# Kernel tuning notes

Hardware: AMD Instinct MI355X
Metric: run time of the kernel (lower is better)

## Reference

```python
import jax, jax.numpy as jnp
from jax import lax
import numpy as np

BN_EPS = 1e-5
LEAKY_SLOPE = 0.1


def _conv(x, w, stride=1):
    # x: [B,Cin,H,W], w: [Cout,Cin,kh,kw], 'same' padding (padding = k//2)
    p = w.shape[2] // 2
    return lax.conv_general_dilated(x, w, (stride, stride), [(p, p), (p, p)],
                                    dimension_numbers=('NCHW', 'OIHW', 'NCHW'))


def _bn(x, g, b, m, v):
    scale = g / jnp.sqrt(v + BN_EPS)
    return x * scale[None, :, None, None] + (b - m * scale)[None, :, None, None]


def _leaky(x):
    return jnp.where(x >= 0, x, LEAKY_SLOPE * x)


def _identity_grid(s, dtype=jnp.float32):
    # F.affine_grid identity, align_corners=True: grid[i,j] = (x_j, y_i), coords in [-1,1]
    xs = jnp.linspace(-1.0, 1.0, s, dtype=dtype)
    gx, gy = jnp.meshgrid(xs, xs)  # gx[i,j]=xs[j], gy[i,j]=xs[i]
    return jnp.stack([gx, gy], axis=-1)[None]  # [1,s,s,2]


def _grid_sample(img, grid):
    # torch.nn.functional.grid_sample, bilinear, align_corners=True, padding_mode='zeros'
    # img: [B,C,H,W], grid: [B,h,w,2] with grid[...,0]=x(width), grid[...,1]=y(height)
    B, C, H, W = img.shape
    x = (grid[..., 0] + 1.0) * 0.5 * (W - 1)
    y = (grid[..., 1] + 1.0) * 0.5 * (H - 1)
    x0f = jnp.floor(x)
    y0f = jnp.floor(y)
    x0 = x0f.astype(jnp.int32)
    y0 = y0f.astype(jnp.int32)
    x1 = x0 + 1
    y1 = y0 + 1
    wx1 = x - x0f
    wx0 = 1.0 - wx1
    wy1 = y - y0f
    wy0 = 1.0 - wy1

    def corner(xi, yi, w):
        m = ((xi >= 0) & (xi < W) & (yi >= 0) & (yi < H)).astype(img.dtype)
        xc = jnp.clip(xi, 0, W - 1)
        yc = jnp.clip(yi, 0, H - 1)
        gath = jax.vmap(lambda im, yy, xx: im[:, yy, xx])(img, yc, xc)  # [B,C,h,w]
        return gath * (w * m)[:, None]

    return (corner(x0, y0, wx0 * wy0) + corner(x1, y0, wx1 * wy0) +
            corner(x0, y1, wx0 * wy1) + corner(x1, y1, wx1 * wy1))


def _correlation(tgt_list, src_list):
    # corr[b, t, h, w] = sum_c tgt[b,c,t] * src[b,c,(h,w)], concat over feature layers (dim 1)
    outs = []
    for t, s in zip(tgt_list, src_list):
        B, C, H, W = t.shape
        c = jnp.einsum('bct,bcs->bts', t.reshape(B, C, H * W), s.reshape(B, C, H * W))
        outs.append(c.reshape(B, H * W, H, W))
    return jnp.concatenate(outs, axis=1)


def _stn_block(corr, i, w0, bn0_g, bn0_b, bn0_m, bn0_v, w1, bn1_g, bn1_b, bn1_m, bn1_v,
               w2, bn2_g, bn2_b, bn2_m, bn2_v, w3, b3):
    # downscale_factor == 1 (output_size == input_size), upsample-to-same-size is identity
    x = _leaky(_bn(_conv(corr, w0[i], stride=1), bn0_g[i], bn0_b[i], bn0_m[i], bn0_v[i]))
    x = _leaky(_bn(_conv(x, w1[i]), bn1_g[i], bn1_b[i], bn1_m[i], bn1_v[i]))
    x = _leaky(_bn(_conv(x, w2[i]), bn2_g[i], bn2_b[i], bn2_m[i], bn2_v[i]))
    x = _conv(x, w3[i]) + b3[i][None, :, None, None]
    return x  # [B,2,S,S]


def setup_inputs() -> dict:
    key = jax.random.key(0)
    ks = iter(jax.random.split(key, 16))
    B, C, S, L, NS = 8, 256, 32, 2, 3  # batch, feat channels, spatial, n feature layers, n scales
    HW = S * S
    d = {
        'src_layer2': jax.random.normal(next(ks), (B, C, S, S), jnp.float32) * 0.1,
        'src_layer3': jax.random.normal(next(ks), (B, C, S, S), jnp.float32) * 0.1,
        'tgt_layer2': jax.random.normal(next(ks), (B, C, S, S), jnp.float32) * 0.1,
        'tgt_layer3': jax.random.normal(next(ks), (B, C, S, S), jnp.float32) * 0.1,
        'w0': jax.random.normal(next(ks), (NS, HW, HW * L, 1, 1), jnp.float32) * 0.02,
        'w1': jax.random.normal(next(ks), (NS, HW // 2, HW, 3, 3), jnp.float32) * 0.02,
        'w2': jax.random.normal(next(ks), (NS, HW // 4, HW // 2, 3, 3), jnp.float32) * 0.02,
        'w3': jax.random.normal(next(ks), (NS, 2, HW // 4, 1, 1), jnp.float32) * 0.02,
        'b3': jnp.zeros((NS, 2), jnp.float32),
    }
    for j, ch in [(0, HW), (1, HW // 2), (2, HW // 4)]:
        d[f'bn{j}_g'] = jnp.ones((NS, ch), jnp.float32)
        d[f'bn{j}_b'] = jnp.zeros((NS, ch), jnp.float32)
        d[f'bn{j}_m'] = jnp.zeros((NS, ch), jnp.float32)
        d[f'bn{j}_v'] = jnp.ones((NS, ch), jnp.float32)
    return d


def reference(src_layer2, src_layer3, tgt_layer2, tgt_layer3,
              w0, bn0_g, bn0_b, bn0_m, bn0_v,
              w1, bn1_g, bn1_b, bn1_m, bn1_v,
              w2, bn2_g, bn2_b, bn2_m, bn2_v,
              w3, b3):
    src = [src_layer2, src_layer3]
    tgt = [tgt_layer2, tgt_layer3]
    S = src_layer2.shape[-1]
    ident = _identity_grid(S, src_layer2.dtype)  # [1,S,S,2]
    params = (w0, bn0_g, bn0_b, bn0_m, bn0_v, w1, bn1_g, bn1_b, bn1_m, bn1_v,
              w2, bn2_g, bn2_b, bn2_m, bn2_v, w3, b3)

    corr = _correlation(tgt, src)
    flow = jnp.transpose(_stn_block(corr, 0, *params), (0, 2, 3, 1)) + ident  # [B,S,S,2]
    n_scales = w0.shape[0]
    for i in range(1, n_scales):
        warped = [_grid_sample(s, flow) for s in src]
        corr = _correlation(tgt, warped)
        flow = flow + jnp.transpose(_stn_block(corr, i, *params), (0, 2, 3, 1))
    return flow
```

## Files before the change

kernel.cpp:

```cpp
#include <hip/hip_runtime.h>
#include <cstdint>
#include <cstddef>


typedef unsigned short u16;
using bf16x8 = __attribute__((ext_vector_type(8))) short;
using f32x4  = __attribute__((ext_vector_type(4))) float;

constexpr float BN_EPS = 1e-5f;
constexpr float SLOPE  = 0.1f;

__device__ __forceinline__ u16 f2bf(float f) {
    union { float f; uint32_t u; } c; c.f = f;
    uint32_t u = c.u;
    return (u16)((u + 0x7fffu + ((u >> 16) & 1u)) >> 16);
}
__device__ __forceinline__ float bf2f(u16 h) {
    union { uint32_t u; float f; } c; c.u = ((uint32_t)h) << 16;
    return c.f;
}

#define MFMA16(a, b, c) __builtin_amdgcn_mfma_f32_16x16x32_bf16(a, b, c, 0, 0, 0)

constexpr size_t OFF_TGT2B  = 0;
constexpr size_t OFF_TGT3B  = 2097152;
constexpr size_t OFF_SRCT2  = 4194304;
constexpr size_t OFF_SRCT3  = 6291456;
constexpr size_t OFF_WARPT2 = 8388608;
constexpr size_t OFF_WARPT3 = 10485760;
constexpr size_t OFF_WPK1   = 12582912;
constexpr size_t OFF_WPK2   = 17301504;
constexpr size_t OFF_EX1    = 18481152;
constexpr size_t OFF_X0P    = 23216128;
constexpr size_t OFF_FLOW   = 32686080;

__global__ __launch_bounds__(256) void cvt_kernel(
    const float* __restrict__ in, u16* __restrict__ out, int n)
{
    int i = (blockIdx.x * 256 + threadIdx.x) * 4;
    if (i + 3 < n) {
        float4 v = *(const float4*)(in + i);
        ushort4 o;
        o.x = f2bf(v.x); o.y = f2bf(v.y); o.z = f2bf(v.z); o.w = f2bf(v.w);
        *(ushort4*)(out + i) = o;
    }
}

__global__ __launch_bounds__(256) void transpose_cvt(
    const float* __restrict__ in, u16* __restrict__ out)
{
    __shared__ float tile[32][33];
    const int s0 = blockIdx.x * 32;
    const int c0 = blockIdx.y * 32;
    const int b  = blockIdx.z;
    const int tid = threadIdx.x;
    const int tx = tid & 31, ty = tid >> 5;
    const float* ib = in + ((size_t)b * 256 + c0) * 1024 + s0;
    #pragma unroll
    for (int r = 0; r < 4; ++r)
        tile[ty + r * 8][tx] = ib[(size_t)(ty + r * 8) * 1024 + tx];
    __syncthreads();
    u16* ob = out + ((size_t)b * 1024 + s0) * 256 + c0;
    #pragma unroll
    for (int r = 0; r < 4; ++r) {
        int s = ty + r * 8;
        ob[(size_t)s * 256 + tx] = f2bf(tile[tx][s]);
    }
}

__global__ __launch_bounds__(256) void pack_conv_w(
    const float* __restrict__ w, u16* __restrict__ out, int COUT, int CIN)
{
    int idx = blockIdx.x * 256 + threadIdx.x;
    if (idx >= COUT * CIN) return;
    int o = idx / CIN, c = idx - o * CIN;
    const float* g = w + (size_t)idx * 9;
    u16* ob = out + (size_t)o * 9 * CIN + c;
    #pragma unroll
    for (int t = 0; t < 9; ++t) ob[(size_t)t * CIN] = f2bf(g[t]);
}

template<int C>
__global__ __launch_bounds__(256) void zero_pads(u16* __restrict__ xP)
{
    constexpr int NC = C / 8;
    int idx = blockIdx.x * 256 + threadIdx.x;
    if (idx >= 8 * 132 * NC) return;
    int c8  = idx & (NC - 1);
    int rem = idx / NC;
    int b = rem / 132, j = rem - b * 132;
    int pos;
    if (j < 34)      pos = j;
    else if (j < 68) pos = 1122 + (j - 34);
    else { int k = j - 68; pos = ((k >> 1) + 1) * 34 + (k & 1) * 33; }
    *(bf16x8*)&xP[((size_t)b * 1156 + pos) * C + c8 * 8] = (bf16x8){0,0,0,0,0,0,0,0};
}

__global__ __launch_bounds__(256) void e_gemm(
    const u16* __restrict__ w0b,
    const u16* __restrict__ tgt2b,
    const u16* __restrict__ tgt3b,
    u16* __restrict__ E)
{
    __shared__ u16 ash[128 * 64];
    __shared__ u16 bsh[128 * 64];
    const int c0 = blockIdx.x * 128;
    const int o0 = blockIdx.y * 128;
    const int b  = blockIdx.z >> 1;
    const int l  = blockIdx.z & 1;
    const u16* tgt = (l == 0 ? tgt2b : tgt3b) + (size_t)b * 262144;
    const int tid = threadIdx.x, lane = tid & 63, wid = tid >> 6;
    const int wm = (wid >> 1) * 64, wn = (wid & 1) * 64;

    f32x4 acc[4][4];
    #pragma unroll
    for (int i = 0; i < 4; ++i)
        #pragma unroll
        for (int j = 0; j < 4; ++j) acc[i][j] = (f32x4){0.f, 0.f, 0.f, 0.f};

    for (int k0 = 0; k0 < 1024; k0 += 64) {
        #pragma unroll
        for (int p = 0; p < 4; ++p) {
            int idx = p * 256 + tid;
            int row = idx >> 3, s = idx & 7;
            *(bf16x8*)&ash[row * 64 + ((s ^ (row & 7)) << 3)] =
                *(const bf16x8*)(w0b + (size_t)(o0 + row) * 2048 + l * 1024 + k0 + s * 8);
            *(bf16x8*)&bsh[row * 64 + ((s ^ (row & 7)) << 3)] =
                *(const bf16x8*)(tgt + (size_t)(c0 + row) * 1024 + k0 + s * 8);
        }
        __syncthreads();
        #pragma unroll
        for (int kk = 0; kk < 2; ++kk) {
            bf16x8 af[4], bfr[4];
            #pragma unroll
            for (int i = 0; i < 4; ++i) {
                int row = wm + i * 16 + (lane & 15);
                int s = kk * 4 + (lane >> 4);
                af[i] = *(const bf16x8*)&ash[row * 64 + ((s ^ (row & 7)) << 3)];
                int rowb = wn + i * 16 + (lane & 15);
                bfr[i] = *(const bf16x8*)&bsh[rowb * 64 + ((s ^ (rowb & 7)) << 3)];
            }
            #pragma unroll
            for (int i = 0; i < 4; ++i)
                #pragma unroll
                for (int j = 0; j < 4; ++j)
                    acc[i][j] = MFMA16(af[i], bfr[j], acc[i][j]);
        }
        __syncthreads();
    }
    u16* Eb = E + ((size_t)blockIdx.z * 1024 + o0) * 256 + c0;
    #pragma unroll
    for (int i = 0; i < 4; ++i)
        #pragma unroll
        for (int j = 0; j < 4; ++j)
            #pragma unroll
            for (int r = 0; r < 4; ++r) {
                int m = wm + i * 16 + ((lane >> 4) << 2) + r;
                int n = wn + j * 16 + (lane & 15);
                Eb[(size_t)m * 256 + n] = f2bf(acc[i][j][r]);
            }
}

__global__ __launch_bounds__(256) void x0_gemm(
    const u16* __restrict__ sA2,
    const u16* __restrict__ sA3,
    const u16* __restrict__ E,
    const float* __restrict__ bng, const float* __restrict__ bnb,
    const float* __restrict__ bnm, const float* __restrict__ bnv,
    u16* __restrict__ x0P)
{
    __shared__ u16 ash[128 * 64];
    __shared__ u16 bsh[128 * 64];
    const int o0 = blockIdx.x * 128;
    const int s0 = blockIdx.y * 128;
    const int b  = blockIdx.z;
    const int tid = threadIdx.x, lane = tid & 63, wid = tid >> 6;
    const int wm = (wid >> 1) * 64, wn = (wid & 1) * 64;

    f32x4 acc[4][4];
    #pragma unroll
    for (int i = 0; i < 4; ++i)
        #pragma unroll
        for (int j = 0; j < 4; ++j) acc[i][j] = (f32x4){0.f, 0.f, 0.f, 0.f};

    for (int kc = 0; kc < 8; ++kc) {
        const int l = kc >> 2;
        const int c0k = (kc & 3) * 64;
        const u16* sa = (l == 0 ? sA2 : sA3) + (size_t)b * 262144;
        const u16* eb = E + (size_t)((b << 1) + l) * 262144;
        #pragma unroll
        for (int p = 0; p < 4; ++p) {
            int idx = p * 256 + tid;
            int row = idx >> 3, s = idx & 7;
            *(bf16x8*)&ash[row * 64 + ((s ^ (row & 7)) << 3)] =
                *(const bf16x8*)(sa + (size_t)(s0 + row) * 256 + c0k + s * 8);
            *(bf16x8*)&bsh[row * 64 + ((s ^ (row & 7)) << 3)] =
                *(const bf16x8*)(eb + (size_t)(o0 + row) * 256 + c0k + s * 8);
        }
        __syncthreads();
        #pragma unroll
        for (int kk = 0; kk < 2; ++kk) {
            bf16x8 af[4], bfr[4];
            #pragma unroll
            for (int i = 0; i < 4; ++i) {
                int row = wm + i * 16 + (lane & 15);
                int s = kk * 4 + (lane >> 4);
                af[i] = *(const bf16x8*)&ash[row * 64 + ((s ^ (row & 7)) << 3)];
                int rowb = wn + i * 16 + (lane & 15);
                bfr[i] = *(const bf16x8*)&bsh[rowb * 64 + ((s ^ (rowb & 7)) << 3)];
            }
            #pragma unroll
            for (int i = 0; i < 4; ++i)
                #pragma unroll
                for (int j = 0; j < 4; ++j)
                    acc[i][j] = MFMA16(af[i], bfr[j], acc[i][j]);
        }
        __syncthreads();
    }
    #pragma unroll
    for (int j = 0; j < 4; ++j) {
        const int o = o0 + wn + j * 16 + (lane & 15);
        const float scv = bng[o] * rsqrtf(bnv[o] + BN_EPS);
        const float shv = bnb[o] - bnm[o] * scv;
        #pragma unroll
        for (int i = 0; i < 4; ++i)
            #pragma unroll
            for (int r = 0; r < 4; ++r) {
                int m = s0 + wm + i * 16 + ((lane >> 4) << 2) + r;
                float t = acc[i][j][r] * scv + shv;
                t = t >= 0.f ? t : SLOPE * t;
                size_t sp = (size_t)b * 1156 + ((m >> 5) + 1) * 34 + (m & 31) + 1;
                x0P[sp * 1024 + o] = f2bf(t);
            }
    }
}

template<int CIN, int COUT, int NT, bool PADOUT>
__global__ __launch_bounds__(256) void conv_gemm(
    const u16* __restrict__ xinP,
    const u16* __restrict__ wpk,
    const float* __restrict__ bng, const float* __restrict__ bnb,
    const float* __restrict__ bnm, const float* __restrict__ bnv,
    u16* __restrict__ xout)
{
    constexpr int NPOS = (NT + 2) * 34;
    constexpr int JT = NT / 2;
    __shared__ u16 ash[9 * 64 * 32];
    __shared__ u16 bsh[NPOS * 36];
    const int o0 = blockIdx.x * 64;
    const int y0 = blockIdx.y * NT;
    const int b  = blockIdx.z;
    const int tid = threadIdx.x, lane = tid & 63, wid = tid >> 6;
    const int wn = wid * (NT * 8);
    const u16* xpb = xinP + ((size_t)b * 1156 + y0 * 34) * CIN;

    f32x4 acc[4][JT];
    #pragma unroll
    for (int i = 0; i < 4; ++i)
        #pragma unroll
        for (int j = 0; j < JT; ++j) acc[i][j] = (f32x4){0.f, 0.f, 0.f, 0.f};

    for (int c0 = 0; c0 < CIN; c0 += 32) {
        #pragma unroll
        for (int p = 0; p < 9; ++p) {
            int idx = p * 256 + tid;
            int row = (idx >> 2) & 63, s = idx & 3;
            *(bf16x8*)&ash[((p * 64 + row) << 5) + ((s ^ ((row >> 1) & 3)) << 3)] =
                *(const bf16x8*)(wpk + ((size_t)(o0 + row) * 9 + p) * CIN + c0 + s * 8);
        }
        for (int idx = tid; idx < NPOS * 4; idx += 256) {
            int pos = idx >> 2, s = idx & 3;
            *(bf16x8*)&bsh[pos * 36 + s * 8] =
                *(const bf16x8*)(xpb + (size_t)pos * CIN + c0 + s * 8);
        }
        __syncthreads();
        #pragma unroll
        for (int t = 0; t < 9; ++t) {
            const int dy = t / 3, dx = t - dy * 3;
            bf16x8 af[4], bfr[JT];
            #pragma unroll
            for (int i = 0; i < 4; ++i) {
                int row = i * 16 + (lane & 15);
                af[i] = *(const bf16x8*)&ash[((t * 64 + row) << 5) +
                                             (((lane >> 4) ^ ((row >> 1) & 3)) << 3)];
            }
            #pragma unroll
            for (int j = 0; j < JT; ++j) {
                int n = wn + j * 16 + (lane & 15);
                int pos = ((n >> 5) + dy) * 34 + (n & 31) + dx;
                bfr[j] = *(const bf16x8*)&bsh[pos * 36 + ((lane >> 4) << 3)];
            }
            #pragma unroll
            for (int i = 0; i < 4; ++i)
                #pragma unroll
                for (int j = 0; j < JT; ++j)
                    acc[i][j] = MFMA16(af[i], bfr[j], acc[i][j]);
        }
        __syncthreads();
    }
    #pragma unroll
    for (int i = 0; i < 4; ++i) {
        float scv[4], shv[4];
        #pragma unroll
        for (int r = 0; r < 4; ++r) {
            int o = o0 + i * 16 + ((lane >> 4) << 2) + r;
            float s = bng[o] * rsqrtf(bnv[o] + BN_EPS);
            scv[r] = s; shv[r] = bnb[o] - bnm[o] * s;
        }
        #pragma unroll
        for (int j = 0; j < JT; ++j) {
            int n = wn + j * 16 + (lane & 15);
            int yg = y0 + (n >> 5), xg = n & 31;
            size_t sp = PADOUT ? ((size_t)b * 1156 + (size_t)(yg + 1) * 34 + xg + 1)
                               : ((size_t)b * 1024 + (size_t)yg * 32 + xg);
            ushort4 pk;
            float t0 = acc[i][j][0] * scv[0] + shv[0]; t0 = t0 >= 0.f ? t0 : SLOPE * t0;
            float t1 = acc[i][j][1] * scv[1] + shv[1]; t1 = t1 >= 0.f ? t1 : SLOPE * t1;
            float t2 = acc[i][j][2] * scv[2] + shv[2]; t2 = t2 >= 0.f ? t2 : SLOPE * t2;
            float t3 = acc[i][j][3] * scv[3] + shv[3]; t3 = t3 >= 0.f ? t3 : SLOPE * t3;
            pk.x = f2bf(t0); pk.y = f2bf(t1); pk.z = f2bf(t2); pk.w = f2bf(t3);
            *(ushort4*)&xout[sp * COUT + o0 + i * 16 + ((lane >> 4) << 2)] = pk;
        }
    }
}

__global__ __launch_bounds__(64) void warp_kernel(
    const u16* __restrict__ srcT,
    const float* __restrict__ flow,
    u16* __restrict__ outT)
{
    const int bs = blockIdx.x;
    const int b = bs >> 10;
    const float fx = flow[(size_t)bs * 2 + 0];
    const float fy = flow[(size_t)bs * 2 + 1];
    const float px = (fx + 1.f) * 15.5f;
    const float py = (fy + 1.f) * 15.5f;
    const float x0f = floorf(px), y0f = floorf(py);
    const int x0 = (int)x0f, y0 = (int)y0f;
    const float wx1 = px - x0f, wx0 = 1.f - wx1;
    const float wy1 = py - y0f, wy0 = 1.f - wy1;
    const int lane = threadIdx.x;
    const u16* sb = srcT + (size_t)b * 262144 + lane * 4;
    float a0 = 0.f, a1 = 0.f, a2 = 0.f, a3 = 0.f;
    #pragma unroll
    for (int cr = 0; cr < 4; ++cr) {
        const int xi = x0 + (cr & 1), yi = y0 + (cr >> 1);
        const float w = (cr == 0 ? wx0 * wy0 : cr == 1 ? wx1 * wy0 :
                         cr == 2 ? wx0 * wy1 : wx1 * wy1);
        if (xi >= 0 && xi < 32 && yi >= 0 && yi < 32) {
            const ushort4 v = *(const ushort4*)(sb + (size_t)(yi * 32 + xi) * 256);
            a0 += w * bf2f(v.x); a1 += w * bf2f(v.y);
            a2 += w * bf2f(v.z); a3 += w * bf2f(v.w);
        }
    }
    ushort4 o;
    o.x = f2bf(a0); o.y = f2bf(a1); o.z = f2bf(a2); o.w = f2bf(a3);
    *(ushort4*)(outT + (size_t)bs * 256 + lane * 4) = o;
}

__global__ __launch_bounds__(256) void conv3_flow(
    const u16* __restrict__ x2T,
    const float* __restrict__ w3s,
    const float* __restrict__ b3s,
    float* __restrict__ flow, int add_ident)
{
    const int widx = blockIdx.x * 4 + (threadIdx.x >> 6);
    const int lane = threadIdx.x & 63;
    const ushort4 v = *(const ushort4*)&x2T[(size_t)widx * 256 + lane * 4];
    float a0 = 0.f, a1 = 0.f;
    const u16* vp = (const u16*)&v;
    #pragma unroll
    for (int j = 0; j < 4; ++j) {
        const float xv = bf2f(vp[j]);
        a0 += xv * w3s[lane * 4 + j];
        a1 += xv * w3s[256 + lane * 4 + j];
    }
    #pragma unroll
    for (int off = 32; off > 0; off >>= 1) {
        a0 += __shfl_down(a0, off);
        a1 += __shfl_down(a1, off);
    }
    if (lane == 0) {
        a0 += b3s[0]; a1 += b3s[1];
        float* f = flow + (size_t)widx * 2;
        if (add_ident) {
            const int s = widx & 1023;
            const int yy = s >> 5, xx = s & 31;
            f[0] = a0 + (-1.f + xx * (2.f / 31.f));
            f[1] = a1 + (-1.f + yy * (2.f / 31.f));
        } else {
            f[0] += a0;
            f[1] += a1;
        }
    }
}

__global__ __launch_bounds__(256) void copy_flow_kernel(
    const float* __restrict__ flow, float* __restrict__ out, int n)
{
    const int i = blockIdx.x * 256 + threadIdx.x;
    if (i < n) out[i] = flow[i];
}

extern "C" void kernel_launch(void* const* d_in, const int* in_sizes, int n_in,
                              void* d_out, int out_size, void* d_ws, size_t ws_size,
                              hipStream_t stream) {
    (void)in_sizes; (void)n_in; (void)ws_size;
    const float* src2 = (const float*)d_in[0];
    const float* src3 = (const float*)d_in[1];
    const float* tgt2 = (const float*)d_in[2];
    const float* tgt3 = (const float*)d_in[3];
    const float* w0   = (const float*)d_in[4];
    const float* w1   = (const float*)d_in[5];
    const float* w2   = (const float*)d_in[6];
    const float* w3   = (const float*)d_in[7];
    const float* b3   = (const float*)d_in[8];
    const float* bn0g = (const float*)d_in[9];
    const float* bn0b = (const float*)d_in[10];
    const float* bn0m = (const float*)d_in[11];
    const float* bn0v = (const float*)d_in[12];
    const float* bn1g = (const float*)d_in[13];
    const float* bn1b = (const float*)d_in[14];
    const float* bn1m = (const float*)d_in[15];
    const float* bn1v = (const float*)d_in[16];
    const float* bn2g = (const float*)d_in[17];
    const float* bn2b = (const float*)d_in[18];
    const float* bn2m = (const float*)d_in[19];
    const float* bn2v = (const float*)d_in[20];

    u16* ws = (u16*)d_ws;
    u16* tgt2b  = ws + OFF_TGT2B;
    u16* tgt3b  = ws + OFF_TGT3B;
    u16* srcT2  = ws + OFF_SRCT2;
    u16* srcT3  = ws + OFF_SRCT3;
    u16* warpT2 = ws + OFF_WARPT2;
    u16* warpT3 = ws + OFF_WARPT3;
    u16* wpk1   = ws + OFF_WPK1;
    u16* wpk2   = ws + OFF_WPK2;
    u16* E      = ws + OFF_EX1;
    u16* x1P    = ws + OFF_EX1;
    u16* x0P    = ws + OFF_X0P;
    u16* w0b    = ws + OFF_X0P;
    u16* x2T    = ws + OFF_WARPT2;
    float* flow = (float*)(ws + OFF_FLOW);

    cvt_kernel<<<2048, 256, 0, stream>>>(tgt2, tgt2b, 2097152);
    cvt_kernel<<<2048, 256, 0, stream>>>(tgt3, tgt3b, 2097152);
    transpose_cvt<<<dim3(32, 8, 8), 256, 0, stream>>>(src2, srcT2);
    transpose_cvt<<<dim3(32, 8, 8), 256, 0, stream>>>(src3, srcT3);

    for (int sc = 0; sc < 3; ++sc) {
        cvt_kernel<<<2048, 256, 0, stream>>>(w0 + (size_t)sc * 2097152, w0b, 2097152);
        pack_conv_w<<<2048, 256, 0, stream>>>(w1 + (size_t)sc * 4718592, wpk1, 512, 1024);
        pack_conv_w<<<512, 256, 0, stream>>>(w2 + (size_t)sc * 1179648, wpk2, 256, 512);

        const u16* a2 = srcT2;
        const u16* a3 = srcT3;
        if (sc > 0) {
            warp_kernel<<<8192, 64, 0, stream>>>(srcT2, flow, warpT2);
            warp_kernel<<<8192, 64, 0, stream>>>(srcT3, flow, warpT3);
            a2 = warpT2; a3 = warpT3;
        }
        e_gemm<<<dim3(2, 8, 16), 256, 0, stream>>>(w0b, tgt2b, tgt3b, E);
        zero_pads<1024><<<528, 256, 0, stream>>>(x0P);
        x0_gemm<<<dim3(8, 8, 8), 256, 0, stream>>>(a2, a3, E,
            bn0g + sc * 1024, bn0b + sc * 1024, bn0m + sc * 1024, bn0v + sc * 1024, x0P);
        zero_pads<512><<<264, 256, 0, stream>>>(x1P);
        conv_gemm<1024, 512, 4, true><<<dim3(8, 8, 8), 256, 0, stream>>>(x0P, wpk1,
            bn1g + sc * 512, bn1b + sc * 512, bn1m + sc * 512, bn1v + sc * 512, x1P);
        conv_gemm<512, 256, 2, false><<<dim3(4, 16, 8), 256, 0, stream>>>(x1P, wpk2,
            bn2g + sc * 256, bn2b + sc * 256, bn2m + sc * 256, bn2v + sc * 256, x2T);
        conv3_flow<<<2048, 256, 0, stream>>>(x2T, w3 + sc * 512, b3 + sc * 2,
                                             flow, sc == 0 ? 1 : 0);
    }
    copy_flow_kernel<<<64, 256, 0, stream>>>(flow, (float*)d_out, out_size);
}
```

Measured before the change: 806.4 us.

## Register-prefetch next K-chunk in conv_gemm and retile conv2 output channels

The conv_gemm main loop now loads the next 32-channel slice of weights and activations into registers while MFMAs run on the current slice in shared memory. This hides global-load latency behind compute, and the trailing barrier is replaced by one at the start of each iteration. A template parameter for the output-channel tile size is added, and conv2 switches from 64x2-row tiles to 32-channel x 4-row tiles. The change raises register pressure, which could reduce occupancy.

After: 736.0 us. -8.7%, faster.

```diff
diff --git a/kernel.cpp b/kernel.cpp
--- a/kernel.cpp
+++ b/kernel.cpp
@@ -235,7 +235,7 @@
     }
 }
 
-template<int CIN, int COUT, int NT, bool PADOUT>
+template<int CIN, int COUT, int MB, int NT, bool PADOUT>
 __global__ __launch_bounds__(256) void conv_gemm(
     const u16* __restrict__ xinP,
     const u16* __restrict__ wpk,
@@ -245,43 +245,85 @@
 {
     constexpr int NPOS = (NT + 2) * 34;
     constexpr int JT = NT / 2;
-    __shared__ u16 ash[9 * 64 * 32];
+    constexpr int WM = MB / 16;
+    constexpr int A_VEC = 9 * MB * 4;
+    constexpr int A_IT  = (A_VEC + 255) / 256;
+    constexpr int B_VEC = NPOS * 4;
+    constexpr int B_IT  = (B_VEC + 255) / 256;
+    __shared__ u16 ash[9 * MB * 32];
     __shared__ u16 bsh[NPOS * 36];
-    const int o0 = blockIdx.x * 64;
+    const int o0 = blockIdx.x * MB;
     const int y0 = blockIdx.y * NT;
     const int b  = blockIdx.z;
     const int tid = threadIdx.x, lane = tid & 63, wid = tid >> 6;
     const int wn = wid * (NT * 8);
     const u16* xpb = xinP + ((size_t)b * 1156 + y0 * 34) * CIN;
 
-    f32x4 acc[4][JT];
-    #pragma unroll
-    for (int i = 0; i < 4; ++i)
+    f32x4 acc[WM][JT];
+    #pragma unroll
+    for (int i = 0; i < WM; ++i)
         #pragma unroll
         for (int j = 0; j < JT; ++j) acc[i][j] = (f32x4){0.f, 0.f, 0.f, 0.f};
 
+    bf16x8 pa[A_IT], pb[B_IT];
+
+    #pragma unroll
+    for (int it = 0; it < A_IT; ++it) {
+        int idx = it * 256 + tid;
+        if (A_VEC % 256 == 0 || idx < A_VEC) {
+            int p = idx / (MB * 4), row = (idx >> 2) % MB, s = idx & 3;
+            pa[it] = *(const bf16x8*)(wpk + ((size_t)(o0 + row) * 9 + p) * CIN + s * 8);
+        }
+    }
+    #pragma unroll
+    for (int it = 0; it < B_IT; ++it) {
+        int idx = it * 256 + tid;
+        if (idx < B_VEC)
+            pb[it] = *(const bf16x8*)(xpb + (size_t)(idx >> 2) * CIN + (idx & 3) * 8);
+    }
+
     for (int c0 = 0; c0 < CIN; c0 += 32) {
-        #pragma unroll
-        for (int p = 0; p < 9; ++p) {
-            int idx = p * 256 + tid;
-            int row = (idx >> 2) & 63, s = idx & 3;
-            *(bf16x8*)&ash[((p * 64 + row) << 5) + ((s ^ ((row >> 1) & 3)) << 3)] =
-                *(const bf16x8*)(wpk + ((size_t)(o0 + row) * 9 + p) * CIN + c0 + s * 8);
-        }
-        for (int idx = tid; idx < NPOS * 4; idx += 256) {
-            int pos = idx >> 2, s = idx & 3;
-            *(bf16x8*)&bsh[pos * 36 + s * 8] =
-                *(const bf16x8*)(xpb + (size_t)pos * CIN + c0 + s * 8);
+        if (c0) __syncthreads();
+        #pragma unroll
+        for (int it = 0; it < A_IT; ++it) {
+            int idx = it * 256 + tid;
+            if (A_VEC % 256 == 0 || idx < A_VEC) {
+                int p = idx / (MB * 4), row = (idx >> 2) % MB, s = idx & 3;
+                *(bf16x8*)&ash[((p * MB + row) << 5) + ((s ^ ((row >> 1) & 3)) << 3)] = pa[it];
+            }
+        }
+        #pragma unroll
+        for (int it = 0; it < B_IT; ++it) {
+            int idx = it * 256 + tid;
+            if (idx < B_VEC)
+                *(bf16x8*)&bsh[(idx >> 2) * 36 + (idx & 3) * 8] = pb[it];
         }
         __syncthreads();
+        if (c0 + 32 < CIN) {
+            const int c1 = c0 + 32;
+            #pragma unroll
+            for (int it = 0; it < A_IT; ++it) {
+                int idx = it * 256 + tid;
+                if (A_VEC % 256 == 0 || idx < A_VEC) {
+                    int p = idx / (MB * 4), row = (idx >> 2) % MB, s = idx & 3;
+                    pa[it] = *(const bf16x8*)(wpk + ((size_t)(o0 + row) * 9 + p) * CIN + c1 + s * 8);
+                }
+            }
+            #pragma unroll
+            for (int it = 0; it < B_IT; ++it) {
+                int idx = it * 256 + tid;
+                if (idx < B_VEC)
+                    pb[it] = *(const bf16x8*)(xpb + (size_t)(idx >> 2) * CIN + c1 + (idx & 3) * 8);
+            }
+        }
         #pragma unroll
         for (int t = 0; t < 9; ++t) {
             const int dy = t / 3, dx = t - dy * 3;
-            bf16x8 af[4], bfr[JT];
-            #pragma unroll
-            for (int i = 0; i < 4; ++i) {
+            bf16x8 af[WM], bfr[JT];
+            #pragma unroll
+            for (int i = 0; i < WM; ++i) {
                 int row = i * 16 + (lane & 15);
-                af[i] = *(const bf16x8*)&ash[((t * 64 + row) << 5) +
+                af[i] = *(const bf16x8*)&ash[((t * MB + row) << 5) +
                                              (((lane >> 4) ^ ((row >> 1) & 3)) << 3)];
             }
             #pragma unroll
@@ -291,15 +333,14 @@
                 bfr[j] = *(const bf16x8*)&bsh[pos * 36 + ((lane >> 4) << 3)];
             }
             #pragma unroll
-            for (int i = 0; i < 4; ++i)
+            for (int i = 0; i < WM; ++i)
                 #pragma unroll
                 for (int j = 0; j < JT; ++j)
                     acc[i][j] = MFMA16(af[i], bfr[j], acc[i][j]);
         }
-        __syncthreads();
-    }
-    #pragma unroll
-    for (int i = 0; i < 4; ++i) {
+    }
+    #pragma unroll
+    for (int i = 0; i < WM; ++i) {
         float scv[4], shv[4];
         #pragma unroll
         for (int r = 0; r < 4; ++r) {
@@ -466,9 +507,9 @@
         x0_gemm<<<dim3(8, 8, 8), 256, 0, stream>>>(a2, a3, E,
             bn0g + sc * 1024, bn0b + sc * 1024, bn0m + sc * 1024, bn0v + sc * 1024, x0P);
         zero_pads<512><<<264, 256, 0, stream>>>(x1P);
-        conv_gemm<1024, 512, 4, true><<<dim3(8, 8, 8), 256, 0, stream>>>(x0P, wpk1,
+        conv_gemm<1024, 512, 64, 4, true><<<dim3(8, 8, 8), 256, 0, stream>>>(x0P, wpk1,
             bn1g + sc * 512, bn1b + sc * 512, bn1m + sc * 512, bn1v + sc * 512, x1P);
-        conv_gemm<512, 256, 2, false><<<dim3(4, 16, 8), 256, 0, stream>>>(x1P, wpk2,
+        conv_gemm<512, 256, 32, 4, false><<<dim3(8, 8, 8), 256, 0, stream>>>(x1P, wpk2,
             bn2g + sc * 256, bn2b + sc * 256, bn2m + sc * 256, bn2v + sc * 256, x2T);
         conv3_flow<<<2048, 256, 0, stream>>>(x2T, w3 + sc * 512, b3 + sc * 2,
                                              flow, sc == 0 ? 1 : 0);
```
